# Performance work log

Measured on AMD Instinct MI355X. Metric: run time of the kernel, lower is better.

Reference implementation:

```python
import jax, jax.numpy as jnp
import numpy as np

DIM = 1024
H = 16
DQK = 64   # head_qk_dim = dim*expand_k / num_heads
DV = 64    # head_v_dim
DIN = 4    # dim_inner (fast-weight rows)
CHUNK = 16
BASE_LR = 1e-3
KS = 4     # short conv kernel size
LN_EPS = 1e-5


def short_conv(x, w):
    """Causal depthwise conv1d (kernel KS) + identity residual.
    x: [b, l, c], w: [c, KS] (tap j multiplies x[t - (KS-1) + j])."""
    b, l, c = x.shape
    xp = jnp.pad(x, ((0, 0), (KS - 1, 0), (0, 0)))
    y = x  # residual: y = conv(x) + x
    for j in range(KS):
        y = y + xp[:, j:j + l, :] * w[None, None, :, j]
    return y


def setup_inputs() -> dict:
    key = jax.random.key(0)
    ks = jax.random.split(key, 16)
    b, l = 4, 2048
    key_dim, value_dim = H * DQK, H * DV
    inp = {
        "hidden_states": jax.random.normal(ks[0], (b, l, DIM), jnp.float32),
        "Wq": jax.random.normal(ks[1], (key_dim, DIM), jnp.float32) / np.sqrt(DIM),
        "Wk": jax.random.normal(ks[2], (key_dim, DIM), jnp.float32) / np.sqrt(DIM),
        "Wv": jax.random.normal(ks[3], (value_dim, DIM), jnp.float32) / np.sqrt(DIM),
        "Wlr": jax.random.normal(ks[4], (2 * H, DIM), jnp.float32) / np.sqrt(DIM),
        "Wo": jax.random.normal(ks[5], (DIM, value_dim), jnp.float32) / np.sqrt(value_dim),
        "Wg": jax.random.normal(ks[6], (DIM, value_dim), jnp.float32) / np.sqrt(value_dim),
        "conv_q": jax.random.normal(ks[7], (key_dim, KS), jnp.float32) / np.sqrt(KS),
        "conv_k": jax.random.normal(ks[8], (key_dim, KS), jnp.float32) / np.sqrt(KS),
        "conv_v": jax.random.normal(ks[9], (value_dim, KS), jnp.float32) / np.sqrt(KS),
        "W_in_init": jax.random.normal(ks[10], (1, DIN, H, DQK), jnp.float32) / np.sqrt(DQK),
        "W_out_init": jax.random.normal(ks[11], (1, DIN, H, DV), jnp.float32) / np.sqrt(DIN),
        "ln_gamma": jnp.ones((DV,), jnp.float32),
        "ln_beta": jnp.zeros((DV,), jnp.float32),
    }
    return inp


def reference(hidden_states, Wq, Wk, Wv, Wlr, Wo, Wg,
              conv_q, conv_k, conv_v, W_in_init, W_out_init, ln_gamma, ln_beta):
    b, l, _ = hidden_states.shape
    scale = 1.0 / np.sqrt(DQK)

    q = short_conv(hidden_states @ Wq.T, conv_q).reshape(b, l, H, DQK)
    k = short_conv(hidden_states @ Wk.T, conv_k).reshape(b, l, H, DQK)
    v = short_conv(hidden_states @ Wv.T, conv_v).reshape(b, l, H, DV)

    lr = jax.nn.softplus(hidden_states @ Wlr.T + BASE_LR).reshape(b, l, H, 2)

    nC = l // CHUNK
    # [nC, b, CHUNK, H, d] for scan over chunks
    qc = q.reshape(b, nC, CHUNK, H, DQK).transpose(1, 0, 2, 3, 4)
    kc = k.reshape(b, nC, CHUNK, H, DQK).transpose(1, 0, 2, 3, 4)
    vc = v.reshape(b, nC, CHUNK, H, DV).transpose(1, 0, 2, 3, 4)
    lrc = lr.reshape(b, nC, CHUNK, H, 2).transpose(1, 0, 2, 3, 4)

    W_in0 = jnp.broadcast_to(W_in_init, (b, DIN, H, DQK))
    W_out0 = jnp.broadcast_to(W_out_init, (b, DIN, H, DV))

    # causal mask: query t (abs pos DIN+t) sees keys j <= DIN+t
    mask = jnp.arange(DIN + CHUNK)[None, :] <= (jnp.arange(CHUNK)[:, None] + DIN)

    def step(carry, xs):
        W_in, W_out = carry
        qch, kch, vch, lrch = xs  # [b, CHUNK, H, d]
        Kf = jnp.concatenate([W_in, kch], axis=1)   # [b, DIN+CHUNK, H, DQK]
        Vf = jnp.concatenate([W_out, vch], axis=1)  # [b, DIN+CHUNK, H, DV]
        s = jnp.einsum('bthd,bshd->bhts', qch, Kf) * scale
        s = jnp.where(mask[None, None], s, -jnp.inf)
        o = jnp.einsum('bhts,bshd->bthd', jax.nn.softmax(s, axis=-1), Vf)

        # fast_kk update rule (non-causal attention, queries = W_in rows)
        g1 = jnp.einsum('bnhd,bchd->bhnc', W_in, kch) * scale
        Grad_out = -jnp.einsum('bhnc,bchd->bnhd', jax.nn.softmax(g1, -1), vch)
        g2 = jnp.einsum('bnhd,bchd->bhnc', W_in, kch * 0.5) * scale
        Grad_in = -jnp.einsum('bhnc,bchd->bnhd', jax.nn.softmax(g2, -1), kch)

        lr_mean = jnp.mean(lrch, axis=1, keepdims=True)  # [b,1,H,2]
        W_in_new = W_in - lr_mean[..., 0:1] * Grad_in
        W_out_new = W_out - lr_mean[..., 1:2] * Grad_out
        return (W_in_new, W_out_new), o

    _, os = jax.lax.scan(step, (W_in0, W_out0), (qc, kc, vc, lrc))
    o = os.transpose(1, 0, 2, 3, 4).reshape(b, l, H, DV)

    # LayerNorm over head_v_dim
    mu = o.mean(-1, keepdims=True)
    var = o.var(-1, keepdims=True)
    o = (o - mu) / jnp.sqrt(var + LN_EPS) * ln_gamma + ln_beta
    o = o.reshape(b, l, H * DV)

    gate = hidden_states @ Wg.T
    return (o * gate) @ Wo.T
```

## Files before the change

### kernel.cpp

```cpp
#include <hip/hip_runtime.h>
#include <hip/hip_bf16.h>
#include <math.h>

#define BATCH 4
#define SEQ   2048
#define DIM   1024
#define NH    16
#define DQK   64
#define DV    64
#define DIN   4
#define CHUNK 16
#define NC    128
#define KS    4
#define TOK   (BATCH*SEQ)
#define SCALE 0.125f
#define BASE_LR 1e-3f
#define LN_EPS 1e-5f
#define K3    3072

typedef float f32x4 __attribute__((ext_vector_type(4)));
typedef short s16x8 __attribute__((ext_vector_type(8)));

__device__ __forceinline__ unsigned short f2bf(float f) {
    unsigned u = __float_as_uint(f);
    u += 0x7fffu + ((u >> 16) & 1u);
    return (unsigned short)(u >> 16);
}
__device__ __forceinline__ float bf2f(unsigned short h) {
    return __uint_as_float(((unsigned)h) << 16);
}

__device__ __forceinline__ void gload_lds16(const void* g, void* l) {
    __builtin_amdgcn_global_load_lds(
        (const __attribute__((address_space(1))) void*)g,
        (__attribute__((address_space(3))) void*)l, 16, 0, 0);
}

__global__ __launch_bounds__(256) void split_bf16_kernel(
    const float* __restrict__ X, unsigned short* __restrict__ Y,
    int rows, int wmode)
{
    const int idx = blockIdx.x * 256 + threadIdx.x;
    if (idx >= rows * (DIM / 4)) return;
    const int r  = idx >> 8;
    const int c4 = (idx & 255) << 2;

    float4 x = *(const float4*)(X + (size_t)r * DIM + c4);
    ushort4 hv, lv;
    hv.x = f2bf(x.x); lv.x = f2bf(x.x - bf2f(hv.x));
    hv.y = f2bf(x.y); lv.y = f2bf(x.y - bf2f(hv.y));
    hv.z = f2bf(x.z); lv.z = f2bf(x.z - bf2f(hv.z));
    hv.w = f2bf(x.w); lv.w = f2bf(x.w - bf2f(hv.w));

    const size_t rb = (size_t)r * K3;
    *(ushort4*)(Y + rb + c4)        = hv;
    *(ushort4*)(Y + rb + 1024 + c4) = wmode ? lv : hv;
    *(ushort4*)(Y + rb + 2048 + c4) = wmode ? hv : lv;
}

__global__ __launch_bounds__(256) void gemm_mfma_qkvg(
    const unsigned short* __restrict__ A, const unsigned short* __restrict__ B,
    float* __restrict__ Cq, float* __restrict__ Ck,
    float* __restrict__ Cv, float* __restrict__ Cg)
{
    __shared__ __align__(16) unsigned short sA[128 * 64];
    __shared__ __align__(16) unsigned short sB[128 * 64];

    const int tid  = threadIdx.x;
    const int lane = tid & 63;
    const int wav  = tid >> 6;

    const int nbx = gridDim.x;
    const int nwg = nbx * gridDim.y;
    int flat = blockIdx.x + blockIdx.y * nbx;
    const int per = nwg >> 3;
    flat = (flat & 7) * per + (flat >> 3);
    const int m0 = (flat / nbx) * 128;
    const int n0 = (flat % nbx) * 128;

    const int wm = (wav >> 1) * 64;
    const int wn = (wav & 1) * 64;

    f32x4 acc[4][4] = {};

    const int fbase = wav * 64 + lane;
    const int lrow  = lane & 15;
    const int g     = lane >> 4;

    for (int kt = 0; kt < K3; kt += 64) {
        __syncthreads();
#pragma unroll
        for (int i = 0; i < 4; ++i) {
            const int f  = fbase + i * 256;
            const int r  = f >> 3;
            const int c  = (f & 7) ^ (r & 7);
            const size_t go = (size_t)r * K3 + kt + c * 8;
            char* lb = (char*)sA + (wav * 64 + i * 256) * 16;
            gload_lds16(A + (size_t)m0 * K3 + go, lb);
        }
#pragma unroll
        for (int i = 0; i < 4; ++i) {
            const int f  = fbase + i * 256;
            const int r  = f >> 3;
            const int c  = (f & 7) ^ (r & 7);
            const size_t go = (size_t)r * K3 + kt + c * 8;
            char* lb = (char*)sB + (wav * 64 + i * 256) * 16;
            gload_lds16(B + (size_t)n0 * K3 + go, lb);
        }
        __syncthreads();

#pragma unroll
        for (int ks = 0; ks < 2; ++ks) {
            const int cbase = ks * 4 + g;
            s16x8 af[4], bfr[4];
#pragma unroll
            for (int mi = 0; mi < 4; ++mi) {
                const int r  = wm + mi * 16 + lrow;
                const int cs = cbase ^ (r & 7);
                af[mi] = *(const s16x8*)((const char*)sA + r * 128 + cs * 16);
            }
#pragma unroll
            for (int ni = 0; ni < 4; ++ni) {
                const int r  = wn + ni * 16 + lrow;
                const int cs = cbase ^ (r & 7);
                bfr[ni] = *(const s16x8*)((const char*)sB + r * 128 + cs * 16);
            }
#pragma unroll
            for (int mi = 0; mi < 4; ++mi)
#pragma unroll
                for (int ni = 0; ni < 4; ++ni)
                    acc[mi][ni] = __builtin_amdgcn_mfma_f32_16x16x32_bf16(
                        af[mi], bfr[ni], acc[mi][ni], 0, 0, 0);
        }
    }

    const int nblk = n0 >> 10;
    float* __restrict__ Co = (nblk == 0) ? Cq : (nblk == 1) ? Ck
                           : (nblk == 2) ? Cv : Cg;
    const int nc0 = (n0 & 1023) + wn;
    const int lcol = lane & 15;
    const int lq   = lane >> 4;
#pragma unroll
    for (int mi = 0; mi < 4; ++mi)
#pragma unroll
        for (int ni = 0; ni < 4; ++ni)
#pragma unroll
            for (int r = 0; r < 4; ++r) {
                const int m = m0 + wm + mi * 16 + lq * 4 + r;
                const int n = nc0 + ni * 16 + lcol;
                Co[(size_t)m * DIM + n] = acc[mi][ni][r];
            }
}

__global__ __launch_bounds__(256) void gemm_mfma_bt(
    const unsigned short* __restrict__ A, const unsigned short* __restrict__ B,
    float* __restrict__ C, int M, int N)
{
    __shared__ __align__(16) unsigned short sA[128 * 64];
    __shared__ __align__(16) unsigned short sB[128 * 64];

    const int tid  = threadIdx.x;
    const int lane = tid & 63;
    const int wav  = tid >> 6;

    const int nbx = gridDim.x;
    const int nwg = nbx * gridDim.y;
    int flat = blockIdx.x + blockIdx.y * nbx;
    const int per = nwg >> 3;
    flat = (flat & 7) * per + (flat >> 3);
    const int m0 = (flat / nbx) * 128;
    const int n0 = (flat % nbx) * 128;

    const int wm = (wav >> 1) * 64;
    const int wn = (wav & 1) * 64;

    f32x4 acc[4][4] = {};

    const int fbase = wav * 64 + lane;
    const int lrow  = lane & 15;
    const int g     = lane >> 4;

    for (int kt = 0; kt < K3; kt += 64) {
        __syncthreads();
#pragma unroll
        for (int i = 0; i < 4; ++i) {
            const int f  = fbase + i * 256;
            const int r  = f >> 3;
            const int c  = (f & 7) ^ (r & 7);
            const size_t go = (size_t)r * K3 + kt + c * 8;
            char* lb = (char*)sA + (wav * 64 + i * 256) * 16;
            gload_lds16(A + (size_t)m0 * K3 + go, lb);
        }
#pragma unroll
        for (int i = 0; i < 4; ++i) {
            const int f  = fbase + i * 256;
            const int r  = f >> 3;
            const int c  = (f & 7) ^ (r & 7);
            const size_t go = (size_t)r * K3 + kt + c * 8;
            char* lb = (char*)sB + (wav * 64 + i * 256) * 16;
            gload_lds16(B + (size_t)n0 * K3 + go, lb);
        }
        __syncthreads();

#pragma unroll
        for (int ks = 0; ks < 2; ++ks) {
            const int cbase = ks * 4 + g;
            s16x8 af[4], bfr[4];
#pragma unroll
            for (int mi = 0; mi < 4; ++mi) {
                const int r  = wm + mi * 16 + lrow;
                const int cs = cbase ^ (r & 7);
                af[mi] = *(const s16x8*)((const char*)sA + r * 128 + cs * 16);
            }
#pragma unroll
            for (int ni = 0; ni < 4; ++ni) {
                const int r  = wn + ni * 16 + lrow;
                const int cs = cbase ^ (r & 7);
                bfr[ni] = *(const s16x8*)((const char*)sB + r * 128 + cs * 16);
            }
#pragma unroll
            for (int mi = 0; mi < 4; ++mi)
#pragma unroll
                for (int ni = 0; ni < 4; ++ni)
                    acc[mi][ni] = __builtin_amdgcn_mfma_f32_16x16x32_bf16(
                        af[mi], bfr[ni], acc[mi][ni], 0, 0, 0);
        }
    }

    const int lcol = lane & 15;
    const int lq   = lane >> 4;
#pragma unroll
    for (int mi = 0; mi < 4; ++mi)
#pragma unroll
        for (int ni = 0; ni < 4; ++ni)
#pragma unroll
            for (int r = 0; r < 4; ++r) {
                const int m = m0 + wm + mi * 16 + lq * 4 + r;
                const int n = n0 + wn + ni * 16 + lcol;
                C[(size_t)m * N + n] = acc[mi][ni][r];
            }
}

#define GBM 128
#define GBN 128
#define GBK 8

__global__ __launch_bounds__(256) void gemm_nt_f32(
    const float* __restrict__ A, const float* __restrict__ B,
    float* __restrict__ C, int M, int N, int K)
{
    __shared__ float As[GBK][GBM + 4];
    __shared__ float Bs[GBK][GBN + 4];

    const int tid = threadIdx.x;
    const int m0 = blockIdx.y * GBM;
    const int n0 = blockIdx.x * GBN;
    const int la_m = tid >> 1;
    const int la_k = (tid & 1) << 2;
    const int tm = tid >> 4;
    const int tn = tid & 15;

    float acc[8][8] = {};

    const float* Arow = A + (size_t)(m0 + la_m) * K + la_k;
    const float* Brow = B + (size_t)(n0 + la_m) * K + la_k;
    const bool bvalid = (n0 + la_m) < N;

    for (int k0 = 0; k0 < K; k0 += GBK) {
        float4 av = *(const float4*)(Arow + k0);
        float4 bv = make_float4(0.f, 0.f, 0.f, 0.f);
        if (bvalid) bv = *(const float4*)(Brow + k0);

        __syncthreads();
        As[la_k + 0][la_m] = av.x; As[la_k + 1][la_m] = av.y;
        As[la_k + 2][la_m] = av.z; As[la_k + 3][la_m] = av.w;
        Bs[la_k + 0][la_m] = bv.x; Bs[la_k + 1][la_m] = bv.y;
        Bs[la_k + 2][la_m] = bv.z; Bs[la_k + 3][la_m] = bv.w;
        __syncthreads();

#pragma unroll
        for (int k = 0; k < GBK; ++k) {
            float4 a0 = *(const float4*)&As[k][tm * 8];
            float4 a1 = *(const float4*)&As[k][tm * 8 + 4];
            float4 b0 = *(const float4*)&Bs[k][tn * 8];
            float4 b1 = *(const float4*)&Bs[k][tn * 8 + 4];
            float a[8] = {a0.x, a0.y, a0.z, a0.w, a1.x, a1.y, a1.z, a1.w};
            float b[8] = {b0.x, b0.y, b0.z, b0.w, b1.x, b1.y, b1.z, b1.w};
#pragma unroll
            for (int i = 0; i < 8; ++i)
#pragma unroll
                for (int j = 0; j < 8; ++j)
                    acc[i][j] += a[i] * b[j];
        }
    }

#pragma unroll
    for (int i = 0; i < 8; ++i) {
        const int m = m0 + tm * 8 + i;
#pragma unroll
        for (int j = 0; j < 8; ++j) {
            const int n = n0 + tn * 8 + j;
            if (n < N) C[(size_t)m * N + n] = acc[i][j];
        }
    }
}

__global__ __launch_bounds__(256) void conv_res_kernel(
    const float* __restrict__ x, const float* __restrict__ w,
    float* __restrict__ y)
{
    const int tid = blockIdx.x * blockDim.x + threadIdx.x;
    if (tid >= TOK * 256) return;
    const int c4  = (tid & 255) << 2;
    const int row = tid >> 8;
    const int t   = row & (SEQ - 1);

    const float* xp = x + (size_t)row * DIM + c4;
    float4 acc = *(const float4*)xp;
    float4 w0 = *(const float4*)(w + (c4 + 0) * 4);
    float4 w1 = *(const float4*)(w + (c4 + 1) * 4);
    float4 w2 = *(const float4*)(w + (c4 + 2) * 4);
    float4 w3 = *(const float4*)(w + (c4 + 3) * 4);

#pragma unroll
    for (int j = 0; j < 4; ++j) {
        const int tt = t - 3 + j;
        if (tt >= 0) {
            float4 xv = *(const float4*)(xp + (j - 3) * DIM);
            acc.x += xv.x * ((&w0.x)[j]);
            acc.y += xv.y * ((&w1.x)[j]);
            acc.z += xv.z * ((&w2.x)[j]);
            acc.w += xv.w * ((&w3.x)[j]);
        }
    }
    *(float4*)(y + (size_t)row * DIM + c4) = acc;
}

__global__ __launch_bounds__(256) void lrmean_kernel(
    const float* __restrict__ lrpre, float* __restrict__ lrm)
{
    const int idx = blockIdx.x * blockDim.x + threadIdx.x;
    if (idx >= BATCH * NC * NH * 2) return;
    const int j = idx & 1;
    const int h = (idx >> 1) & 15;
    const int c = (idx >> 5) & 127;
    const int b = idx >> 12;

    float s = 0.f;
#pragma unroll
    for (int i = 0; i < CHUNK; ++i) {
        float x = lrpre[((size_t)b * SEQ + c * CHUNK + i) * 32 + h * 2 + j] + BASE_LR;
        s += fmaxf(x, 0.f) + log1pf(expf(-fabsf(x)));
    }
    lrm[idx] = s * (1.f / CHUNK);
}

__global__ __launch_bounds__(128) void state_scan_kernel(
    const float* __restrict__ kconv, const float* __restrict__ vconv,
    const float* __restrict__ lrm,
    const float* __restrict__ win_init, const float* __restrict__ wout_init,
    float* __restrict__ wst_in, float* __restrict__ wst_out)
{
    const int bh  = blockIdx.x;
    const int b   = bh >> 4, h = bh & 15;
    const int tid = threadIdx.x;
    const int wv  = tid >> 6;
    const int d   = tid & 63;

    __shared__ __align__(16) float sW[DIN][68];
    __shared__ __align__(16) float sK[CHUNK][68];
    __shared__ __align__(16) float sP1[2][DIN][16];
    __shared__ __align__(16) float sP2[2][DIN][16];
    __shared__ float sLR[NC * 2];

    const float* __restrict__ xin  = wv ? vconv     : kconv;
    const float* __restrict__ wini = wv ? wout_init : win_init;
    float*       __restrict__ wst  = wv ? wst_out   : wst_in;

    float W[DIN];
#pragma unroll
    for (int n = 0; n < DIN; ++n) W[n] = wini[(n * NH + h) * 64 + d];

    sLR[tid * 2 + 0] = lrm[(((size_t)b * NC + tid) * NH + h) * 2 + 0];
    sLR[tid * 2 + 1] = lrm[(((size_t)b * NC + tid) * NH + h) * 2 + 1];

    const int gn = d >> 4;
    const int gc = d & 15;

    float xa[CHUNK], xb[CHUNK];
    const size_t base00 = (size_t)b * SEQ * DIM + h * 64 + d;
#pragma unroll
    for (int i = 0; i < CHUNK; ++i) xa[i] = xin[base00 + (size_t)i * DIM];
    asm volatile("s_waitcnt lgkmcnt(0)" ::: "memory");

#define SCAN_STEP(c, XA, XB)                                                   \
    {                                                                          \
        const int pb = (c) & 1;                                                \
        if ((c) + 1 < NC) {                                                    \
            const size_t basen = base00 + (size_t)(((c) + 1) * CHUNK) * DIM;   \
            _Pragma("unroll")                                                  \
            for (int i = 0; i < CHUNK; ++i)                                    \
                XB[i] = xin[basen + (size_t)i * DIM];                          \
        }                                                                      \
        const size_t wofs = (((size_t)bh * NC + (c)) * DIN) * 64 + d;          \
        _Pragma("unroll")                                                      \
        for (int n = 0; n < DIN; ++n) wst[wofs + n * 64] = W[n];               \
        if (wv == 0) {                                                         \
            _Pragma("unroll")                                                  \
            for (int i = 0; i < CHUNK; ++i) sK[i][d] = XA[i];                  \
            _Pragma("unroll")                                                  \
            for (int n = 0; n < DIN; ++n) sW[n][d] = W[n];                     \
            asm volatile("s_waitcnt lgkmcnt(0)" ::: "memory");                 \
            float p0 = 0.f, p1 = 0.f, p2 = 0.f, p3 = 0.f;                      \
            _Pragma("unroll")                                                  \
            for (int q = 0; q < 4; ++q) {                                      \
                const int o = q * 16;                                          \
                float4 w0 = *(const float4*)&sW[gn][o + 0];                    \
                float4 k0 = *(const float4*)&sK[gc][o + 0];                    \
                float4 w1 = *(const float4*)&sW[gn][o + 4];                    \
                float4 k1 = *(const float4*)&sK[gc][o + 4];                    \
                float4 w2 = *(const float4*)&sW[gn][o + 8];                    \
                float4 k2 = *(const float4*)&sK[gc][o + 8];                    \
                float4 w3 = *(const float4*)&sW[gn][o + 12];                   \
                float4 k3 = *(const float4*)&sK[gc][o + 12];                   \
                p0 += w0.x*k0.x; p0 += w0.y*k0.y; p0 += w0.z*k0.z; p0 += w0.w*k0.w; \
                p1 += w1.x*k1.x; p1 += w1.y*k1.y; p1 += w1.z*k1.z; p1 += w1.w*k1.w; \
                p2 += w2.x*k2.x; p2 += w2.y*k2.y; p2 += w2.z*k2.z; p2 += w2.w*k2.w; \
                p3 += w3.x*k3.x; p3 += w3.y*k3.y; p3 += w3.z*k3.z; p3 += w3.w*k3.w; \
            }                                                                  \
            const float g1 = ((p0 + p1) + (p2 + p3)) * SCALE;                  \
            float m = g1;                                                      \
            _Pragma("unroll")                                                  \
            for (int mk = 8; mk >= 1; mk >>= 1)                                \
                m = fmaxf(m, __shfl_xor(m, mk, 16));                           \
            const float e1 = expf(g1 - m);                                     \
            const float rr = sqrtf(e1);                 \
            float s1 = e1, s2 = rr;                                            \
            _Pragma("unroll")                                                  \
            for (int mk = 8; mk >= 1; mk >>= 1) {                              \
                s1 += __shfl_xor(s1, mk, 16);                                  \
                s2 += __shfl_xor(s2, mk, 16);                                  \
            }                                                                  \
            sP1[pb][gn][gc] = e1 / s1;                                         \
            sP2[pb][gn][gc] = rr / s2;                                         \
            asm volatile("s_waitcnt lgkmcnt(0)" ::: "memory");                 \
        }                                                                      \
        __builtin_amdgcn_s_barrier();                                          \
        const float lr = sLR[(c) * 2 + wv];                                    \
        const float (*P)[16] = wv ? sP1[pb] : sP2[pb];                         \
        _Pragma("unroll")                                                      \
        for (int n = 0; n < DIN; ++n) {                                        \
            float4 q0 = *(const float4*)&P[n][0];                              \
            float4 q1 = *(const float4*)&P[n][4];                              \
            float4 q2 = *(const float4*)&P[n][8];                              \
            float4 q3 = *(const float4*)&P[n][12];                             \
            float t0 = q0.x*XA[0];  t0 += q0.y*XA[1];                          \
            t0 += q0.z*XA[2];       t0 += q0.w*XA[3];                          \
            float t1 = q1.x*XA[4];  t1 += q1.y*XA[5];                          \
            t1 += q1.z*XA[6];       t1 += q1.w*XA[7];                          \
            float t2 = q2.x*XA[8];  t2 += q2.y*XA[9];                          \
            t2 += q2.z*XA[10];      t2 += q2.w*XA[11];                         \
            float t3 = q3.x*XA[12]; t3 += q3.y*XA[13];                         \
            t3 += q3.z*XA[14];      t3 += q3.w*XA[15];                         \
            W[n] += lr * ((t0 + t1) + (t2 + t3));                              \
        }                                                                      \
    }

    for (int c = 0; c < NC; c += 2) {
        SCAN_STEP(c,     xa, xb);
        SCAN_STEP(c + 1, xb, xa);
    }
#undef SCAN_STEP
}

__global__ __launch_bounds__(64) void attn_kernel(
    const float* __restrict__ qconv, const float* __restrict__ kconv,
    const float* __restrict__ vconv,
    const float* __restrict__ wst_in, const float* __restrict__ wst_out,
    const float* __restrict__ gate,
    const float* __restrict__ gamma, const float* __restrict__ beta,
    float* __restrict__ og)
{
    const int blk = blockIdx.x;
    const int c  = blk & (NC - 1);
    const int bh = blk >> 7;
    const int h = bh & 15, b = bh >> 4;
    const int d = threadIdx.x;

    __shared__ float sQ[CHUNK][65];
    __shared__ float sKf[DIN + CHUNK][65];
    __shared__ float sS[CHUNK][21];
    __shared__ float sO[CHUNK][65];
    __shared__ float sMu[CHUNK], sRs[CHUNK];

    float vf[DIN + CHUNK];

    const size_t wofs = (size_t)blk * (DIN * 64) + d;
#pragma unroll
    for (int n = 0; n < DIN; ++n) {
        sKf[n][d] = wst_in [wofs + n * 64];
        vf[n]     = wst_out[wofs + n * 64];
    }
    const size_t base = ((size_t)b * SEQ + c * CHUNK) * DIM + h * 64 + d;
#pragma unroll
    for (int i = 0; i < CHUNK; ++i) {
        sQ[i][d]        = qconv[base + (size_t)i * DIM];
        sKf[DIN + i][d] = kconv[base + (size_t)i * DIM];
        vf[DIN + i]     = vconv[base + (size_t)i * DIM];
    }
    __syncthreads();

#pragma unroll
    for (int r = 0; r < 5; ++r) {
        const int p = d + 64 * r;
        const int t = p / 20, j = p % 20;
        float dot = 0.f;
#pragma unroll
        for (int dd = 0; dd < 64; ++dd) dot += sQ[t][dd] * sKf[j][dd];
        float s = dot * SCALE;
        if (j >= DIN && (j - DIN) > t) s = -3.0e38f;
        sS[t][j] = s;
    }
    __syncthreads();

    if (d < CHUNK) {
        float m = -3.0e38f;
#pragma unroll
        for (int j = 0; j < DIN + CHUNK; ++j) m = fmaxf(m, sS[d][j]);
        float e[DIN + CHUNK];
        float sum = 0.f;
#pragma unroll
        for (int j = 0; j < DIN + CHUNK; ++j) { e[j] = expf(sS[d][j] - m); sum += e[j]; }
        const float inv = 1.f / sum;
#pragma unroll
        for (int j = 0; j < DIN + CHUNK; ++j) sS[d][j] = e[j] * inv;
    }
    __syncthreads();

#pragma unroll
    for (int t = 0; t < CHUNK; ++t) {
        float o = 0.f;
#pragma unroll
        for (int j = 0; j < DIN + CHUNK; ++j) o += sS[t][j] * vf[j];
        sO[t][d] = o;
    }
    __syncthreads();

    if (d < CHUNK) {
        float su = 0.f, sq = 0.f;
#pragma unroll
        for (int dd = 0; dd < 64; ++dd) { float x = sO[d][dd]; su += x; sq += x * x; }
        float mu = su * (1.f / 64.f);
        float var = sq * (1.f / 64.f) - mu * mu;
        sMu[d] = mu;
        sRs[d] = rsqrtf(var + LN_EPS);
    }
    __syncthreads();

    const float gm = gamma[d], bt = beta[d];
#pragma unroll
    for (int t = 0; t < CHUNK; ++t) {
        float val = (sO[t][d] - sMu[t]) * sRs[t] * gm + bt;
        float gval = gate[base + (size_t)t * DIM];
        og[base + (size_t)t * DIM] = val * gval;
    }
}

extern "C" void kernel_launch(void* const* d_in, const int* in_sizes, int n_in,
                              void* d_out, int out_size, void* d_ws, size_t ws_size,
                              hipStream_t stream)
{
    const float* hid   = (const float*)d_in[0];
    const float* Wq    = (const float*)d_in[1];
    const float* Wk    = (const float*)d_in[2];
    const float* Wv    = (const float*)d_in[3];
    const float* Wlr   = (const float*)d_in[4];
    const float* Wo    = (const float*)d_in[5];
    const float* Wg    = (const float*)d_in[6];
    const float* cq    = (const float*)d_in[7];
    const float* ck    = (const float*)d_in[8];
    const float* cv    = (const float*)d_in[9];
    const float* wini  = (const float*)d_in[10];
    const float* wouti = (const float*)d_in[11];
    const float* lng   = (const float*)d_in[12];
    const float* lnb   = (const float*)d_in[13];
    float* out = (float*)d_out;

    float* ws = (float*)d_ws;
    const size_t DSZ = (size_t)TOK * DIM;
    float* qraw  = ws;
    float* kraw  = qraw + DSZ;
    float* vraw  = kraw + DSZ;
    float* gatb  = vraw + DSZ;
    float* lrpre = gatb + DSZ;
    float* lrm   = lrpre + (size_t)TOK * 32;
    float* wsti  = lrm   + BATCH * NC * NH * 2;
    float* wsto  = wsti  + (size_t)BATCH * NH * NC * DIN * 64;
    unsigned short* Abuf = (unsigned short*)(wsto + (size_t)BATCH * NH * NC * DIN * 64);
    unsigned short* Bbuf = Abuf + (size_t)TOK * K3;
    float* spar = (float*)Bbuf;

    float* qv = spar;
    float* kv = qraw;
    float* vv = kraw;

    const dim3 blk256(256);
    const dim3 fused_grid(32, 64);
    const dim3 out_grid(8, 64);
    const dim3 gemm_grid_lr(1, TOK / GBM);
    const int conv_blocks = (TOK * 256 + 255) / 256;

    split_bf16_kernel<<<TOK, blk256, 0, stream>>>(hid, Abuf, TOK, 0);
    split_bf16_kernel<<<1024, blk256, 0, stream>>>(Wq, Bbuf,                       1024, 1);
    split_bf16_kernel<<<1024, blk256, 0, stream>>>(Wk, Bbuf + (size_t)1024 * K3,   1024, 1);
    split_bf16_kernel<<<1024, blk256, 0, stream>>>(Wv, Bbuf + (size_t)2048 * K3,   1024, 1);
    split_bf16_kernel<<<1024, blk256, 0, stream>>>(Wg, Bbuf + (size_t)3072 * K3,   1024, 1);

    gemm_mfma_qkvg<<<fused_grid, blk256, 0, stream>>>(Abuf, Bbuf, qraw, kraw, vraw, gatb);

    conv_res_kernel<<<conv_blocks, blk256, 0, stream>>>(qraw, cq, spar);
    conv_res_kernel<<<conv_blocks, blk256, 0, stream>>>(kraw, ck, qraw);
    conv_res_kernel<<<conv_blocks, blk256, 0, stream>>>(vraw, cv, kraw);

    gemm_nt_f32<<<gemm_grid_lr, blk256, 0, stream>>>(hid, Wlr, lrpre, TOK, 32, DIM);
    lrmean_kernel<<<(BATCH * NC * NH * 2 + 255) / 256, blk256, 0, stream>>>(lrpre, lrm);

    state_scan_kernel<<<BATCH * NH, 128, 0, stream>>>(kv, vv, lrm, wini, wouti, wsti, wsto);
    attn_kernel<<<BATCH * NH * NC, 64, 0, stream>>>(qv, kv, vv, wsti, wsto,
                                                    gatb, lng, lnb, qv);

    split_bf16_kernel<<<TOK, blk256, 0, stream>>>(qv, Abuf, TOK, 0);
    split_bf16_kernel<<<1024, blk256, 0, stream>>>(Wo, Bbuf, 1024, 1);
    gemm_mfma_bt<<<out_grid, blk256, 0, stream>>>(Abuf, Bbuf, out, TOK, DIM);
}
```

Before: 917.8 us.

## Use 256x256 tiles with double-buffered LDS pipeline in fused QKVG GEMM

The fused QKVG GEMM goes from 128x128 tiles with 4 waves to 256x256 tiles with 8 waves. Each wave now holds an 8x4 grid of MFMA accumulators. Shared memory is double-buffered so the next k-tile's global-to-LDS loads overlap the MFMA work on the current tile, using explicit vmcnt waits, raw barriers and setprio. This is meant to raise arithmetic intensity and hide load latency in the largest GEMM, at the cost of more registers and LDS per block (128KB) and fewer blocks in the grid.

New measurement: 886.1 us. -3.5%, faster.

```diff
diff --git a/kernel.cpp b/kernel.cpp
--- a/kernel.cpp
+++ b/kernel.cpp
@@ -58,80 +58,97 @@
     *(ushort4*)(Y + rb + 2048 + c4) = wmode ? hv : lv;
 }
 
-__global__ __launch_bounds__(256) void gemm_mfma_qkvg(
+__global__ __launch_bounds__(512, 2) void gemm_mfma_qkvg(
     const unsigned short* __restrict__ A, const unsigned short* __restrict__ B,
     float* __restrict__ Cq, float* __restrict__ Ck,
     float* __restrict__ Cv, float* __restrict__ Cg)
 {
-    __shared__ __align__(16) unsigned short sA[128 * 64];
-    __shared__ __align__(16) unsigned short sB[128 * 64];
+    __shared__ __align__(16) unsigned short sA[2][256 * 64];
+    __shared__ __align__(16) unsigned short sB[2][256 * 64];
 
     const int tid  = threadIdx.x;
     const int lane = tid & 63;
-    const int wav  = tid >> 6;
+    const int wid  = tid >> 6;
 
     const int nbx = gridDim.x;
     const int nwg = nbx * gridDim.y;
     int flat = blockIdx.x + blockIdx.y * nbx;
     const int per = nwg >> 3;
     flat = (flat & 7) * per + (flat >> 3);
-    const int m0 = (flat / nbx) * 128;
-    const int n0 = (flat % nbx) * 128;
-
-    const int wm = (wav >> 1) * 64;
-    const int wn = (wav & 1) * 64;
-
-    f32x4 acc[4][4] = {};
-
-    const int fbase = wav * 64 + lane;
-    const int lrow  = lane & 15;
-    const int g     = lane >> 4;
-
-    for (int kt = 0; kt < K3; kt += 64) {
-        __syncthreads();
-#pragma unroll
-        for (int i = 0; i < 4; ++i) {
-            const int f  = fbase + i * 256;
-            const int r  = f >> 3;
-            const int c  = (f & 7) ^ (r & 7);
-            const size_t go = (size_t)r * K3 + kt + c * 8;
-            char* lb = (char*)sA + (wav * 64 + i * 256) * 16;
-            gload_lds16(A + (size_t)m0 * K3 + go, lb);
-        }
-#pragma unroll
-        for (int i = 0; i < 4; ++i) {
-            const int f  = fbase + i * 256;
-            const int r  = f >> 3;
-            const int c  = (f & 7) ^ (r & 7);
-            const size_t go = (size_t)r * K3 + kt + c * 8;
-            char* lb = (char*)sB + (wav * 64 + i * 256) * 16;
-            gload_lds16(B + (size_t)n0 * K3 + go, lb);
-        }
-        __syncthreads();
-
+    const int m0 = (flat / nbx) * 256;
+    const int n0 = (flat % nbx) * 256;
+
+    const int wm = (wid >> 2) * 128;
+    const int wn = (wid & 3) * 64;
+
+    f32x4 acc[8][4] = {};
+
+    const int lrow = lane & 15;
+    const int g    = lane >> 4;
+
+#define STAGE256(kt, db)                                                       \
+    {                                                                          \
+        _Pragma("unroll")                                                      \
+        for (int i = 0; i < 4; ++i) {                                          \
+            const int f = tid + i * 512;                 \
+            const int r = f >> 3;                        \
+            const int c = (f & 7) ^ (r & 7);             \
+            gload_lds16(A + (size_t)(m0 + r) * K3 + (kt) * 64 + c * 8,         \
+                        (char*)sA[db] + (wid * 64 + i * 512) * 16);            \
+        }                                                                      \
+        _Pragma("unroll")                                                      \
+        for (int i = 0; i < 4; ++i) {                                          \
+            const int f = tid + i * 512;                                       \
+            const int r = f >> 3;                                              \
+            const int c = (f & 7) ^ (r & 7);                                   \
+            gload_lds16(B + (size_t)(n0 + r) * K3 + (kt) * 64 + c * 8,         \
+                        (char*)sB[db] + (wid * 64 + i * 512) * 16);            \
+        }                                                                      \
+    }
+
+    STAGE256(0, 0);
+    STAGE256(1, 1);
+
+    const int NT = K3 / 64;
+    for (int t = 0; t < NT; ++t) {
+        const int cur = t & 1;
+        if (t < NT - 1) asm volatile("s_waitcnt vmcnt(8)" ::: "memory");
+        else            asm volatile("s_waitcnt vmcnt(0)" ::: "memory");
+        __builtin_amdgcn_s_barrier();
+        asm volatile("" ::: "memory");
+
+        const unsigned short* __restrict__ pA = sA[cur];
+        const unsigned short* __restrict__ pB = sB[cur];
+        __builtin_amdgcn_s_setprio(1);
 #pragma unroll
         for (int ks = 0; ks < 2; ++ks) {
             const int cbase = ks * 4 + g;
-            s16x8 af[4], bfr[4];
-#pragma unroll
-            for (int mi = 0; mi < 4; ++mi) {
+            s16x8 af[8], bfr[4];
+#pragma unroll
+            for (int mi = 0; mi < 8; ++mi) {
                 const int r  = wm + mi * 16 + lrow;
                 const int cs = cbase ^ (r & 7);
-                af[mi] = *(const s16x8*)((const char*)sA + r * 128 + cs * 16);
+                af[mi] = *(const s16x8*)((const char*)pA + r * 128 + cs * 16);
             }
 #pragma unroll
             for (int ni = 0; ni < 4; ++ni) {
                 const int r  = wn + ni * 16 + lrow;
                 const int cs = cbase ^ (r & 7);
-                bfr[ni] = *(const s16x8*)((const char*)sB + r * 128 + cs * 16);
+                bfr[ni] = *(const s16x8*)((const char*)pB + r * 128 + cs * 16);
             }
 #pragma unroll
-            for (int mi = 0; mi < 4; ++mi)
+            for (int mi = 0; mi < 8; ++mi)
 #pragma unroll
                 for (int ni = 0; ni < 4; ++ni)
                     acc[mi][ni] = __builtin_amdgcn_mfma_f32_16x16x32_bf16(
                         af[mi], bfr[ni], acc[mi][ni], 0, 0, 0);
         }
+        __builtin_amdgcn_s_setprio(0);
+
+        asm volatile("" ::: "memory");
+        __builtin_amdgcn_s_barrier();
+        asm volatile("" ::: "memory");
+        if (t + 2 < NT) STAGE256(t + 2, cur);
     }
 
     const int nblk = n0 >> 10;
@@ -141,7 +158,7 @@
     const int lcol = lane & 15;
     const int lq   = lane >> 4;
 #pragma unroll
-    for (int mi = 0; mi < 4; ++mi)
+    for (int mi = 0; mi < 8; ++mi)
 #pragma unroll
         for (int ni = 0; ni < 4; ++ni)
 #pragma unroll
@@ -150,6 +167,7 @@
                 const int n = nc0 + ni * 16 + lcol;
                 Co[(size_t)m * DIM + n] = acc[mi][ni][r];
             }
+#undef STAGE256
 }
 
 __global__ __launch_bounds__(256) void gemm_mfma_bt(
@@ -605,7 +623,7 @@
     float* vv = kraw;
 
     const dim3 blk256(256);
-    const dim3 fused_grid(32, 64);
+    const dim3 fused_grid(16, 32);
     const dim3 out_grid(8, 64);
     const dim3 gemm_grid_lr(1, TOK / GBM);
     const int conv_blocks = (TOK * 256 + 255) / 256;
@@ -616,7 +634,7 @@
     split_bf16_kernel<<<1024, blk256, 0, stream>>>(Wv, Bbuf + (size_t)2048 * K3,   1024, 1);
     split_bf16_kernel<<<1024, blk256, 0, stream>>>(Wg, Bbuf + (size_t)3072 * K3,   1024, 1);
 
-    gemm_mfma_qkvg<<<fused_grid, blk256, 0, stream>>>(Abuf, Bbuf, qraw, kraw, vraw, gatb);
+    gemm_mfma_qkvg<<<fused_grid, 512, 0, stream>>>(Abuf, Bbuf, qraw, kraw, vraw, gatb);
 
     conv_res_kernel<<<conv_blocks, blk256, 0, stream>>>(qraw, cq, spar);
     conv_res_kernel<<<conv_blocks, blk256, 0, stream>>>(kraw, ck, qraw);
```
